# Kernel optimization log

Measured on AMD Instinct MI355X. Metric: run time of the kernel, lower is better.

## Reference

```python
import jax, jax.numpy as jnp
import numpy as np

R_CUT = 5.0
L_MAX = 3
N_MAX = (8, 7, 6, 5)  # n_max per angular order l (Laplacian-eigenstate-like, shrinking with l)
EPS = 1e-12


def _radial_basis(r):
    """r: [E] -> [E, N_MAX[0]] sine radial basis with smooth cosine cutoff.
    R_n(r) = f_cut(r) * sin((n+1) pi r / r_cut) / r, n = 0..n_max-1."""
    n = jnp.arange(1, N_MAX[0] + 1, dtype=r.dtype)  # (n+1)
    fcut = jnp.where(r < R_CUT, 0.5 * (jnp.cos(jnp.pi * r / R_CUT) + 1.0), 0.0)
    rb = jnp.sin(n[None, :] * (jnp.pi / R_CUT) * r[:, None]) / (r[:, None] + EPS)
    return rb * fcut[:, None]


def _spherical_harmonics(v, r):
    """v: [E,3], r: [E] -> tuple of real SH arrays ([E,1],[E,3],[E,5],[E,7]), m = -l..l."""
    ir = 1.0 / (r + EPS)
    x, y, z = v[:, 0] * ir, v[:, 1] * ir, v[:, 2] * ir
    pi = np.pi
    x2, y2, z2 = x * x, y * y, z * z
    # l = 0
    y0 = jnp.full_like(r, 0.5 * np.sqrt(1.0 / pi))[:, None]
    # l = 1
    c1 = np.sqrt(3.0 / (4.0 * pi))
    y1 = jnp.stack([c1 * y, c1 * z, c1 * x], axis=-1)
    # l = 2
    y2b = jnp.stack([
        0.5 * np.sqrt(15.0 / pi) * x * y,
        0.5 * np.sqrt(15.0 / pi) * y * z,
        0.25 * np.sqrt(5.0 / pi) * (2.0 * z2 - x2 - y2),
        0.5 * np.sqrt(15.0 / pi) * x * z,
        0.25 * np.sqrt(15.0 / pi) * (x2 - y2),
    ], axis=-1)
    # l = 3
    y3b = jnp.stack([
        0.25 * np.sqrt(35.0 / (2.0 * pi)) * y * (3.0 * x2 - y2),
        0.5 * np.sqrt(105.0 / pi) * x * y * z,
        0.25 * np.sqrt(21.0 / (2.0 * pi)) * y * (4.0 * z2 - x2 - y2),
        0.25 * np.sqrt(7.0 / pi) * z * (2.0 * z2 - 3.0 * x2 - 3.0 * y2),
        0.25 * np.sqrt(21.0 / (2.0 * pi)) * x * (4.0 * z2 - x2 - y2),
        0.25 * np.sqrt(105.0 / pi) * z * (x2 - y2),
        0.25 * np.sqrt(35.0 / (2.0 * pi)) * x * (x2 - 3.0 * y2),
    ], axis=-1)
    return (y0, y1, y2b, y3b)


def setup_inputs() -> dict:
    key = jax.random.key(0)
    E = 1_000_000
    vectors = 1.5 * jax.random.normal(key, (E, 3), dtype=jnp.float32)
    return {"vectors": vectors}


def reference(vectors):
    # vectors: [E, 3] bare cartesian edge vectors
    r = jnp.sqrt(jnp.sum(vectors * vectors, axis=-1))  # [E]
    rb = _radial_basis(r)                               # [E, N_MAX[0]]
    sh = _spherical_harmonics(vectors, r)               # per-l [E, 2l+1]
    # vector_expansion_l = radial_l[:, None, :] * sh_l[:, :, None] -> [E, 2l+1, n_max_l]
    blocks = tuple(sh[l][:, :, None] * rb[:, None, :N_MAX[l]] for l in range(L_MAX + 1))
    return blocks
```

## Files before the change

kernel.cpp:

```cpp
#include <hip/hip_runtime.h>
#include <math.h>


#define RCUT 5.0f
#define EPSF 1e-12f

typedef float fx4 __attribute__((ext_vector_type(4)));

__device__ __forceinline__ void radial(float rr, float ir, float rb[8]) {
  float theta = (3.14159265358979323846f / RCUT) * rr;
  float s = __sinf(theta);
  float c = __cosf(theta);
  float fcut = (rr < RCUT) ? 0.5f * (c + 1.0f) : 0.0f;
  float g = fcut * ir;
  float twoc = 2.0f * c;
  float sp = 0.0f, sn = s;
  rb[0] = sn * g;
#pragma unroll
  for (int n = 1; n < 8; ++n) {
    float s2 = twoc * sn - sp;
    sp = sn;
    sn = s2;
    rb[n] = sn * g;
  }
}

template <int L>
__device__ __forceinline__ void do_section(const float* __restrict__ v,
                                           float* __restrict__ secbase, int E,
                                           int task, fx4* __restrict__ l4,
                                           int lane, int wave) {
  constexpr int M = 2 * L + 1;
  constexpr int NM = 8 - L;
  constexpr int S = M * NM;
  const long long e0 = ((long long)task * 4 + wave) * 64;
  if (e0 >= E) return;
  const bool fullwave = (e0 + 64 <= (long long)E);
  const int e = (int)e0 + lane;
  const bool valid = e < E;

  float x = 0.0f, y = 0.0f, z = 0.0f;
  if (valid) {
    x = v[3 * (size_t)e + 0];
    y = v[3 * (size_t)e + 1];
    z = v[3 * (size_t)e + 2];
  }
  float rr = sqrtf(x * x + y * y + z * z);
  float ir = 1.0f / (rr + EPSF);
  float rb[8];
  radial(rr, ir, rb);

  float ux = x * ir, uy = y * ir, uz = z * ir;
  float xx = ux * ux, yy = uy * uy, zz = uz * uz;

  float sh[M];
  if constexpr (L == 1) {
    const float c1 = 0.48860251190291992f;
    sh[0] = c1 * uy;
    sh[1] = c1 * uz;
    sh[2] = c1 * ux;
  } else if constexpr (L == 2) {
    const float c2a = 1.09254843059207907f;
    const float c2b = 0.31539156525252001f;
    const float c2c = 0.54627421529603953f;
    sh[0] = c2a * ux * uy;
    sh[1] = c2a * uy * uz;
    sh[2] = c2b * (2.0f * zz - xx - yy);
    sh[3] = c2a * ux * uz;
    sh[4] = c2c * (xx - yy);
  } else {
    const float c3a = 0.59004358992664352f;
    const float c3b = 2.89061144264055405f;
    const float c3c = 0.45704579946446574f;
    const float c3d = 0.37317633259011546f;
    const float c3e = 1.44530572132027702f;
    sh[0] = c3a * uy * (3.0f * xx - yy);
    sh[1] = c3b * ux * uy * uz;
    sh[2] = c3c * uy * (4.0f * zz - xx - yy);
    sh[3] = c3d * uz * (2.0f * zz - 3.0f * xx - 3.0f * yy);
    sh[4] = c3c * ux * (4.0f * zz - xx - yy);
    sh[5] = c3e * uz * (xx - yy);
    sh[6] = c3a * ux * (xx - 3.0f * yy);
  }

  float vals[S];
#pragma unroll
  for (int m = 0; m < M; ++m)
#pragma unroll
    for (int n = 0; n < NM; ++n) vals[m * NM + n] = sh[m] * rb[n];

  if (fullwave) {
    float* lw = reinterpret_cast<float*>(l4);
#pragma unroll
    for (int i = 0; i < S; ++i) lw[lane * S + i] = vals[i];
    fx4* g4 = reinterpret_cast<fx4*>(secbase + (size_t)e0 * S);
    constexpr int NF4 = 16 * S;
    constexpr int NITER = (NF4 + 63) / 64;
#pragma unroll
    for (int it = 0; it < NITER; ++it) {
      int k = lane + it * 64;
      if ((NF4 % 64 == 0) || k < NF4)
        __builtin_nontemporal_store(l4[k], &g4[k]);
    }
  } else if (valid) {
    float* o = secbase + (size_t)e * S;
#pragma unroll
    for (int i = 0; i < S; ++i) o[i] = vals[i];
  }
}

__global__ __launch_bounds__(256) void vexp_fused(const float* __restrict__ v,
                                                  float* __restrict__ out,
                                                  int E, int gsec) {
  __shared__ fx4 lbuf[4][560];
  const int bid = blockIdx.x;
  const int lane = threadIdx.x & 63;
  const int wave = threadIdx.x >> 6;
  const size_t E_ = (size_t)E;

  if (bid < gsec) {
    const long long n4 = 2LL * E;
    const float y0c = 0.28209479177387814f;
#pragma unroll
    for (int k = 0; k < 2; ++k) {
      long long t = (long long)bid * 256 + threadIdx.x + (long long)k * gsec * 256;
      if (t < n4) {
        long long e = t >> 1;
        int half = (int)(t & 1);
        float x = v[3 * e + 0], y = v[3 * e + 1], z = v[3 * e + 2];
        float rr = sqrtf(x * x + y * y + z * z);
        float ir = 1.0f / (rr + EPSF);
        float rb[8];
        radial(rr, ir, rb);
        int o = 4 * half;
        fx4 val = {y0c * rb[o], y0c * rb[o + 1], y0c * rb[o + 2],
                   y0c * rb[o + 3]};
        __builtin_nontemporal_store(val, &reinterpret_cast<fx4*>(out)[t]);
      }
    }
  } else if (bid < 2 * gsec) {
    do_section<1>(v, out + 8 * E_, E, bid - gsec, lbuf[wave], lane, wave);
  } else if (bid < 3 * gsec) {
    do_section<2>(v, out + 29 * E_, E, bid - 2 * gsec, lbuf[wave], lane, wave);
  } else {
    do_section<3>(v, out + 59 * E_, E, bid - 3 * gsec, lbuf[wave], lane, wave);
  }
}

extern "C" void kernel_launch(void* const* d_in, const int* in_sizes, int n_in,
                              void* d_out, int out_size, void* d_ws, size_t ws_size,
                              hipStream_t stream) {
  const float* v = (const float*)d_in[0];
  float* out = (float*)d_out;
  int E = in_sizes[0] / 3;
  int waves = (E + 63) / 64;
  int gsec = (waves + 3) / 4;
  vexp_fused<<<4 * gsec, 256, 0, stream>>>(v, out, E, gsec);
}
```

Before: 73.35 us.

## Process four tasks per block with software-prefetched edge loads

Each block now handles four consecutive wave-tasks per section instead of one. It loads the next task's edge vector before computing and storing the current one, so input loads overlap with compute and the LDS-staged stores. The l=0 section switches to a grid-stride loop with a runtime iteration count. This cuts the grid size by four and launch/block overhead, at the cost of less parallelism per block and possible tail imbalance. It also reuses the same LDS buffer across iterations without a barrier between store passes.

```diff
diff --git a/kernel.cpp b/kernel.cpp
--- a/kernel.cpp
+++ b/kernel.cpp
@@ -26,25 +26,17 @@
 }
 
 template <int L>
-__device__ __forceinline__ void do_section(const float* __restrict__ v,
-                                           float* __restrict__ secbase, int E,
-                                           int task, fx4* __restrict__ l4,
-                                           int lane, int wave) {
+__device__ __forceinline__ void emit_task(float x, float y, float z,
+                                          long long e0, int E,
+                                          float* __restrict__ secbase,
+                                          fx4* __restrict__ l4, int lane) {
   constexpr int M = 2 * L + 1;
   constexpr int NM = 8 - L;
   constexpr int S = M * NM;
-  const long long e0 = ((long long)task * 4 + wave) * 64;
-  if (e0 >= E) return;
   const bool fullwave = (e0 + 64 <= (long long)E);
   const int e = (int)e0 + lane;
   const bool valid = e < E;
 
-  float x = 0.0f, y = 0.0f, z = 0.0f;
-  if (valid) {
-    x = v[3 * (size_t)e + 0];
-    y = v[3 * (size_t)e + 1];
-    z = v[3 * (size_t)e + 2];
-  }
   float rr = sqrtf(x * x + y * y + z * z);
   float ir = 1.0f / (rr + EPSF);
   float rb[8];
@@ -109,21 +101,61 @@
   }
 }
 
+template <int L>
+__device__ __forceinline__ void do_sec_pipe(const float* __restrict__ v,
+                                            float* __restrict__ secbase, int E,
+                                            int t0, int ntask,
+                                            fx4* __restrict__ l4, int lane,
+                                            int wave) {
+  float cx = 0.0f, cy = 0.0f, cz = 0.0f;
+  {
+    long long e0 = ((long long)t0 * 4 + wave) * 64;
+    int e = (int)e0 + lane;
+    if (e0 < E && e < E) {
+      cx = v[3 * (size_t)e + 0];
+      cy = v[3 * (size_t)e + 1];
+      cz = v[3 * (size_t)e + 2];
+    }
+  }
+#pragma unroll
+  for (int j = 0; j < 4; ++j) {
+    int task = t0 + j;
+    long long e0 = ((long long)task * 4 + wave) * 64;
+    float nx = 0.0f, ny = 0.0f, nz = 0.0f;
+    if (j < 3) {
+      long long en0 = ((long long)(task + 1) * 4 + wave) * 64;
+      int en = (int)en0 + lane;
+      if (en0 < E && en < E) {
+        nx = v[3 * (size_t)en + 0];
+        ny = v[3 * (size_t)en + 1];
+        nz = v[3 * (size_t)en + 2];
+      }
+    }
+    if (task < ntask && e0 < E)
+      emit_task<L>(cx, cy, cz, e0, E, secbase, l4, lane);
+    cx = nx;
+    cy = ny;
+    cz = nz;
+  }
+}
+
 __global__ __launch_bounds__(256) void vexp_fused(const float* __restrict__ v,
                                                   float* __restrict__ out,
-                                                  int E, int gsec) {
+                                                  int E, int nb, int ntask,
+                                                  int iters0) {
   __shared__ fx4 lbuf[4][560];
   const int bid = blockIdx.x;
   const int lane = threadIdx.x & 63;
   const int wave = threadIdx.x >> 6;
   const size_t E_ = (size_t)E;
 
-  if (bid < gsec) {
+  if (bid < nb) {
     const long long n4 = 2LL * E;
+    const long long stride = (long long)nb * 256;
+    long long t = (long long)bid * 256 + threadIdx.x;
     const float y0c = 0.28209479177387814f;
-#pragma unroll
-    for (int k = 0; k < 2; ++k) {
-      long long t = (long long)bid * 256 + threadIdx.x + (long long)k * gsec * 256;
+#pragma unroll 2
+    for (int it = 0; it < iters0; ++it) {
       if (t < n4) {
         long long e = t >> 1;
         int half = (int)(t & 1);
@@ -137,13 +169,17 @@
                    y0c * rb[o + 3]};
         __builtin_nontemporal_store(val, &reinterpret_cast<fx4*>(out)[t]);
       }
+      t += stride;
     }
-  } else if (bid < 2 * gsec) {
-    do_section<1>(v, out + 8 * E_, E, bid - gsec, lbuf[wave], lane, wave);
-  } else if (bid < 3 * gsec) {
-    do_section<2>(v, out + 29 * E_, E, bid - 2 * gsec, lbuf[wave], lane, wave);
+  } else if (bid < 2 * nb) {
+    do_sec_pipe<1>(v, out + 8 * E_, E, (bid - nb) * 4, ntask, lbuf[wave],
+                   lane, wave);
+  } else if (bid < 3 * nb) {
+    do_sec_pipe<2>(v, out + 29 * E_, E, (bid - 2 * nb) * 4, ntask, lbuf[wave],
+                   lane, wave);
   } else {
-    do_section<3>(v, out + 59 * E_, E, bid - 3 * gsec, lbuf[wave], lane, wave);
+    do_sec_pipe<3>(v, out + 59 * E_, E, (bid - 3 * nb) * 4, ntask, lbuf[wave],
+                   lane, wave);
   }
 }
 
@@ -154,6 +190,9 @@
   float* out = (float*)d_out;
   int E = in_sizes[0] / 3;
   int waves = (E + 63) / 64;
-  int gsec = (waves + 3) / 4;
-  vexp_fused<<<4 * gsec, 256, 0, stream>>>(v, out, E, gsec);
+  int ntask = (waves + 3) / 4;
+  int nb = (ntask + 3) / 4;
+  long long stride = (long long)nb * 256;
+  int iters0 = (int)((2LL * E + stride - 1) / stride);
+  vexp_fused<<<4 * nb, 256, 0, stream>>>(v, out, E, nb, ntask, iters0);
 }
```

Result: slower. 77.43 us (+5.6%).
